# Optimization experiments

Measured on AMD Instinct MI355X. Metric: run time of the kernel, lower is better.

## Reference

```python
import jax, jax.numpy as jnp
import numpy as np

B, N, K, C = 8, 4096, 16, 64
OUT = [128, 128, 128]
BN_EPS = 1e-3


def setup_inputs() -> dict:
    key = jax.random.key(0)
    ks = jax.random.split(key, 8)
    inp = {
        "points1": jax.random.normal(ks[0], (B, 3, N), jnp.float32),
        "points2": jax.random.normal(ks[1], (B, 3, N), jnp.float32),
        "features1": jax.random.normal(ks[2], (B, C, N), jnp.float32),
        "features2": jax.random.normal(ks[3], (B, C, N), jnp.float32),
    }
    dims = [2 * C + 3] + OUT  # [131, 128, 128, 128]
    for i in range(len(OUT)):
        kw = jax.random.fold_in(ks[4], i)
        inp[f"W{i}"] = jax.random.normal(kw, (dims[i + 1], dims[i]), jnp.float32) / np.sqrt(dims[i]).astype(np.float32)
        inp[f"b{i}"] = jnp.zeros((dims[i + 1],), jnp.float32)
        inp[f"gamma{i}"] = jnp.ones((dims[i + 1],), jnp.float32)
        inp[f"beta{i}"] = jnp.zeros((dims[i + 1],), jnp.float32)
    return inp


def _knn_group(points2, points1, features2):
    # points*: [B, 3, N].  For each query in points1, find K nearest in points2.
    d = jnp.sum((points1[:, :, :, None] - points2[:, :, None, :]) ** 2, axis=1)  # [B, Nq, Ns]
    _, idx = jax.lax.top_k(-d, K)  # [B, Nq, K]
    idx_b = idx[:, None, :, :]  # [B, 1, Nq, K] broadcasts over channel dim
    xyz_g = jnp.take_along_axis(points2[:, :, None, :], idx_b, axis=3)      # [B, 3, Nq, K]
    rel_xyz = xyz_g - points1[:, :, :, None]                                # relative coords
    feat_g = jnp.take_along_axis(features2[:, :, None, :], idx_b, axis=3)  # [B, C, Nq, K]
    return jnp.concatenate([rel_xyz, feat_g], axis=1)  # [B, C+3, Nq, K]


def _conv_bn_relu(x, W, b, gamma, beta):
    # 1x1 conv == per-position channel matmul; BN in training mode (batch stats, biased var)
    x = jnp.einsum('oc,bcnk->bonk', W, x) + b[None, :, None, None]
    mu = jnp.mean(x, axis=(0, 2, 3), keepdims=True)
    var = jnp.var(x, axis=(0, 2, 3), keepdims=True)
    x = (x - mu) * jax.lax.rsqrt(var + BN_EPS)
    x = x * gamma[None, :, None, None] + beta[None, :, None, None]
    return jax.nn.relu(x)


def reference(points1, points2, features1, features2,
              W0, b0, gamma0, beta0,
              W1, b1, gamma1, beta1,
              W2, b2, gamma2, beta2):
    g = _knn_group(points2, points1, features2)                       # [B, C+3, N, K]
    f1 = jnp.broadcast_to(features1[:, :, :, None], (B, C, N, K))     # expand over neighbors
    x = jnp.concatenate([g, f1], axis=1)                              # [B, 2C+3, N, K]
    x = _conv_bn_relu(x, W0, b0, gamma0, beta0)
    x = _conv_bn_relu(x, W1, b1, gamma1, beta1)
    x = _conv_bn_relu(x, W2, b2, gamma2, beta2)
    return jnp.max(x, axis=3)                                         # [B, OUT[-1], N]
```

## Files before the change

### kernel.cpp

```cpp
#include <hip/hip_runtime.h>
#include <hip/hip_bf16.h>

#define B_ 8
#define N_ 4096
#define K_ 16
#define C_ 64
#define NK_ (N_*K_)
#define M_ (B_*N_*K_)
#define BN_EPS_ 0.001f
#define Q_ (B_*N_)
#define NB1_ (M_/128)
#define CAP_ 48

typedef short bf16x8 __attribute__((ext_vector_type(8)));
typedef float f32x4 __attribute__((ext_vector_type(4)));

static __device__ __forceinline__ unsigned pk2bf(float a, float b) {
  union { __hip_bfloat162 h; unsigned u; } c;
  c.h = __float22bfloat162_rn(make_float2(a, b));
  return c.u;
}
static __device__ __forceinline__ unsigned short f2bf1(float x) {
  union { __hip_bfloat16 h; unsigned short u; } c;
  c.h = __float2bfloat16(x);
  return c.u;
}

static __device__ __forceinline__ float knn_key(float ax, float ay, float az, float4 c) {
  float dx = ax - c.x, dy = ay - c.y, dz = az - c.z;
  return __fadd_rn(__fadd_rn(__fmul_rn(dx, dx), __fmul_rn(dy, dy)), __fmul_rn(dz, dz));
}

__global__ __launch_bounds__(256) void prep_kernel(
    const float* __restrict__ p1, const float* __restrict__ p2,
    const float* __restrict__ W1, const float* __restrict__ W2,
    const float* __restrict__ W0,
    float4* __restrict__ p1f4, float4* __restrict__ p2f4,
    unsigned short* __restrict__ W1b, unsigned short* __restrict__ W2b,
    float* __restrict__ w0at, float* __restrict__ stats, int* __restrict__ done) {
  int blk = blockIdx.x, tid = threadIdx.x;
  if (blk < 128) {
    int i = blk * 256 + tid;
    int b = i >> 12, n = i & (N_ - 1);
    const float* base = p1 + (size_t)b * 3 * N_;
    p1f4[i] = make_float4(base[n], base[N_ + n], base[2 * N_ + n], 0.f);
  } else if (blk < 256) {
    int i = (blk - 128) * 256 + tid;
    int b = i >> 12, n = i & (N_ - 1);
    const float* base = p2 + (size_t)b * 3 * N_;
    p2f4[i] = make_float4(base[n], base[N_ + n], base[2 * N_ + n], 0.f);
  } else if (blk < 320) {
    int i = (blk - 256) * 256 + tid;
    W1b[i] = f2bf1(W1[i]);
  } else if (blk < 384) {
    int i = (blk - 320) * 256 + tid;
    W2b[i] = f2bf1(W2[i]);
  } else {
    if (tid < 128)
      for (int d = 0; d < 3; ++d) w0at[d * 128 + tid] = W0[tid * 131 + d];
    for (int i = tid; i < 768; i += 256) stats[i] = 0.f;
    if (tid < 3) done[tid] = 0;
  }
}

__global__ __launch_bounds__(64) void knn_sub(const float4* __restrict__ p1f4,
                                              const float4* __restrict__ p2f4,
                                              float* __restrict__ pvals) {
  int lane = threadIdx.x;
  int blk = blockIdx.x;
  int c = blk & 3;
  int grp = (blk >> 2) & 63;
  int b = blk >> 8;
  int q = (b << 12) + (grp << 6) + lane;
  float4 qv = p1f4[q];
  float ax = qv.x, ay = qv.y, az = qv.z;
  const float4* pb = p2f4 + ((size_t)b << 12) + c * 128;

  float s[16];
  #pragma unroll
  for (int i = 0; i < 16; ++i) s[i] = 3.0e38f;

  #pragma unroll 8
  for (int t = 0; t < 128; ++t) {
    float d = knn_key(ax, ay, az, pb[t]);
    #pragma unroll
    for (int i = 0; i < 15; ++i) s[i] = __builtin_amdgcn_fmed3f(s[i], s[i + 1], d);
    s[15] = fminf(s[15], d);
  }
  #pragma unroll
  for (int i = 0; i < 16; ++i) pvals[(size_t)(c * 16 + i) * Q_ + q] = s[i];
}

__global__ __launch_bounds__(64) void knn_t0(const float* __restrict__ pvals,
                                             float* __restrict__ Tarr) {
  int q = blockIdx.x * 64 + threadIdx.x;
  float s[16];
  #pragma unroll
  for (int i = 0; i < 16; ++i) s[i] = 3.0e38f;
  #pragma unroll 8
  for (int t = 0; t < 64; ++t) {
    float d = pvals[(size_t)t * Q_ + q];
    #pragma unroll
    for (int i = 0; i < 15; ++i) s[i] = __builtin_amdgcn_fmed3f(s[i], s[i + 1], d);
    s[15] = fminf(s[15], d);
  }
  Tarr[q] = s[0];
}

__global__ __launch_bounds__(64) void knn_collect(const float4* __restrict__ p1f4,
                                                  const float4* __restrict__ p2f4,
                                                  const float* __restrict__ Tarr,
                                                  uint2* __restrict__ cbuf,
                                                  int* __restrict__ ccnt) {
  int lane = threadIdx.x;
  int blk = blockIdx.x;
  int c = blk & 7;
  int grp = (blk >> 3) & 63;
  int b = blk >> 9;
  int q = (b << 12) + (grp << 6) + lane;
  float4 qv = p1f4[q];
  float ax = qv.x, ay = qv.y, az = qv.z;
  const float4* pb = p2f4 + ((size_t)b << 12) + c * 512;
  float T = Tarr[q];
  uint2* cq = cbuf + (size_t)q * (8 * CAP_) + c * CAP_;
  int cnt = 0;
  #pragma unroll 4
  for (int t = 0; t < 512; ++t) {
    float d = knn_key(ax, ay, az, pb[t]);
    if (d <= T && cnt < CAP_) {
      cq[cnt] = make_uint2(__float_as_uint(d), c * 512 + t);
      ++cnt;
    }
  }
  ccnt[c * Q_ + q] = cnt;
}

__global__ __launch_bounds__(256) void knn_final(const uint2* __restrict__ cbuf,
                                                 const int* __restrict__ ccnt,
                                                 int* __restrict__ idxout) {
  int lane = threadIdx.x & 63;
  int q = blockIdx.x * 4 + (threadIdx.x >> 6);
  const uint2* cq = cbuf + (size_t)q * (8 * CAP_);

  float key[8], okey[8];
  unsigned kidx[8];
  #pragma unroll
  for (int c = 0; c < 8; ++c) {
    int m = ccnt[c * Q_ + q];
    float k = 3.0e38f; unsigned id = 0;
    if (lane < m) {
      uint2 e = cq[c * CAP_ + lane];
      k = __uint_as_float(e.x); id = e.y;
    }
    key[c] = k; okey[c] = k; kidx[c] = id;
  }

  float T = 3.0e38f;
  for (int r = 0; r < 16; ++r) {
    float lm = key[0]; int ls = 0;
    #pragma unroll
    for (int c = 1; c < 8; ++c) if (key[c] < lm) { lm = key[c]; ls = c; }
    float wm = lm;
    wm = fminf(wm, __shfl_xor(wm, 1));
    wm = fminf(wm, __shfl_xor(wm, 2));
    wm = fminf(wm, __shfl_xor(wm, 4));
    wm = fminf(wm, __shfl_xor(wm, 8));
    wm = fminf(wm, __shfl_xor(wm, 16));
    wm = fminf(wm, __shfl_xor(wm, 32));
    T = wm;
    unsigned long long msk = __ballot(lm == wm);
    int owner = __ffsll((long long)msk) - 1;
    if (lane == owner) key[ls] = 3.0e38f;
  }

  int tot = 0, ob = q * 16;
  #pragma unroll
  for (int c = 0; c < 8; ++c) {
    bool take = (okey[c] <= T);
    unsigned long long msk = __ballot(take);
    int pos = tot + __popcll(msk & ((1ull << lane) - 1ull));
    if (take && pos < 16) idxout[ob + pos] = (int)kidx[c];
    tot += __popcll(msk);
  }
}

__global__ __launch_bounds__(256) void pkern(const float* __restrict__ f,
                                             const float* __restrict__ W0,
                                             const float* __restrict__ bias,
                                             const float4* __restrict__ pf4,
                                             const float* __restrict__ w0at,
                                             float sgn,
                                             float* __restrict__ P, int coff) {
  __shared__ float fx[32 * 65];
  __shared__ __align__(16) float Wl[64 * 132];
  int tid = threadIdx.x;
  int bn0 = blockIdx.x * 32;
  int b = bn0 >> 12, nb0 = bn0 & (N_ - 1);

  for (int u = tid; u < 32 * 64; u += 256) {
    int c = u >> 5, nl = u & 31;
    fx[nl * 65 + c] = f[((size_t)b * C_ + c) * N_ + nb0 + nl];
  }
  for (int u = tid; u < 128 * 64; u += 256) {
    int o = u >> 6, c = u & 63;
    Wl[c * 132 + o] = W0[o * 131 + coff + c];
  }
  __syncthreads();

  int og = tid & 15, np_ = tid >> 4;
  int o0 = og * 8;
  int na = np_ * 2, nb = na + 1;
  float acc0[8], acc1[8];
  #pragma unroll
  for (int j = 0; j < 8; ++j) {
    float bv = bias ? bias[o0 + j] : 0.f;
    acc0[j] = bv; acc1[j] = bv;
  }
  for (int c = 0; c < 64; ++c) {
    float x0 = fx[na * 65 + c], x1 = fx[nb * 65 + c];
    float4 wa = *(const float4*)&Wl[c * 132 + o0];
    float4 wb = *(const float4*)&Wl[c * 132 + o0 + 4];
    float w[8] = {wa.x, wa.y, wa.z, wa.w, wb.x, wb.y, wb.z, wb.w};
    #pragma unroll
    for (int j = 0; j < 8; ++j) {
      acc0[j] = fmaf(x0, w[j], acc0[j]);
      acc1[j] = fmaf(x1, w[j], acc1[j]);
    }
  }
  float4 pa = pf4[bn0 + na], pb_ = pf4[bn0 + nb];
  #pragma unroll
  for (int j = 0; j < 8; ++j) {
    float wx = w0at[o0 + j], wy = w0at[128 + o0 + j], wz = w0at[256 + o0 + j];
    acc0[j] += sgn * (wx * pa.x + wy * pa.y + wz * pa.z);
    acc1[j] += sgn * (wx * pb_.x + wy * pb_.y + wz * pb_.z);
  }
  float* Pa = P + (size_t)(bn0 + na) * 128 + o0;
  float* Pb = P + (size_t)(bn0 + nb) * 128 + o0;
  *(float4*)Pa = make_float4(acc0[0], acc0[1], acc0[2], acc0[3]);
  *(float4*)(Pa + 4) = make_float4(acc0[4], acc0[5], acc0[6], acc0[7]);
  *(float4*)Pb = make_float4(acc1[0], acc1[1], acc1[2], acc1[3]);
  *(float4*)(Pb + 4) = make_float4(acc1[4], acc1[5], acc1[6], acc1[7]);
}

__global__ __launch_bounds__(256) void gstats_kernel(
    const float* __restrict__ A, const float* __restrict__ Bv,
    const int* __restrict__ idx, unsigned short* __restrict__ x0b,
    float* __restrict__ part) {
  __shared__ float sred[4 * 128 * 2];
  int tid = threadIdx.x;
  int R0 = blockIdx.x * 128;
  int b = R0 >> 16;
  int n0 = (R0 & (NK_ - 1)) >> 4;
  int cc = (tid & 15) * 8;
  int r0l = tid >> 4;

  int jj[8];
  #pragma unroll
  for (int p = 0; p < 8; ++p) jj[p] = idx[R0 + r0l + p * 16];

  float ssum[8], ssq[8];
  #pragma unroll
  for (int u = 0; u < 8; ++u) { ssum[u] = 0.f; ssq[u] = 0.f; }

  #pragma unroll
  for (int p = 0; p < 8; ++p) {
    const float* Ar = A + (size_t)((b << 12) + n0 + p) * 128 + cc;
    const float* Br = Bv + (size_t)((b << 12) + jj[p]) * 128 + cc;
    float av[8], bv[8];
    *(float4*)&av[0] = *(const float4*)Ar;  *(float4*)&av[4] = *(const float4*)(Ar + 4);
    *(float4*)&bv[0] = *(const float4*)Br;  *(float4*)&bv[4] = *(const float4*)(Br + 4);
    unsigned pw[4];
    #pragma unroll
    for (int i = 0; i < 4; ++i)
      pw[i] = pk2bf(av[2 * i] + bv[2 * i], av[2 * i + 1] + bv[2 * i + 1]);
    uint4 pk; pk.x = pw[0]; pk.y = pw[1]; pk.z = pw[2]; pk.w = pw[3];
    *(uint4*)(x0b + (size_t)(R0 + r0l + p * 16) * 128 + cc) = pk;
    #pragma unroll
    for (int i = 0; i < 4; ++i) {
      float q0 = __uint_as_float(pw[i] << 16);
      float q1 = __uint_as_float(pw[i] & 0xFFFF0000u);
      ssum[2 * i] += q0;     ssq[2 * i] = fmaf(q0, q0, ssq[2 * i]);
      ssum[2 * i + 1] += q1; ssq[2 * i + 1] = fmaf(q1, q1, ssq[2 * i + 1]);
    }
  }
  int w = tid >> 6, lane = tid & 63;
  #pragma unroll
  for (int u = 0; u < 8; ++u) {
    ssum[u] += __shfl_xor(ssum[u], 16);
    ssum[u] += __shfl_xor(ssum[u], 32);
    ssq[u] += __shfl_xor(ssq[u], 16);
    ssq[u] += __shfl_xor(ssq[u], 32);
  }
  if (lane < 16) {
    #pragma unroll
    for (int u = 0; u < 8; ++u) {
      sred[(w * 128 + lane * 8 + u) * 2] = ssum[u];
      sred[(w * 128 + lane * 8 + u) * 2 + 1] = ssq[u];
    }
  }
  __syncthreads();
  if (tid < 128) {
    float a = 0.f, q2 = 0.f;
    #pragma unroll
    for (int ww = 0; ww < 4; ++ww) {
      a += sred[(ww * 128 + tid) * 2];
      q2 += sred[(ww * 128 + tid) * 2 + 1];
    }
    part[(size_t)blockIdx.x * 256 + tid] = a;
    part[(size_t)blockIdx.x * 256 + 128 + tid] = q2;
  }
}

__global__ __launch_bounds__(256) void reduce_bnfin(
    const float* __restrict__ part, float* __restrict__ statso,
    int* __restrict__ done, const float* __restrict__ gamma,
    const float* __restrict__ beta, float* __restrict__ bnp) {
  __shared__ int lastv;
  int tid = threadIdx.x;
  int r0 = blockIdx.x * 16;
  float a = 0.f;
  #pragma unroll
  for (int i = 0; i < 16; ++i) a += part[(size_t)(r0 + i) * 256 + tid];
  atomicAdd(statso + tid, a);
  __threadfence();
  __syncthreads();
  if (tid == 0) lastv = atomicAdd(done, 1);
  __syncthreads();
  if (lastv == (int)gridDim.x - 1) {
    __threadfence();
    if (tid < 128) {
      float s0 = atomicAdd(statso + tid, 0.f);
      float s1 = atomicAdd(statso + 128 + tid, 0.f);
      const float invM = 1.0f / (float)M_;
      float mean = s0 * invM;
      float var = s1 * invM - mean * mean;
      float s = gamma[tid] * rsqrtf(var + BN_EPS_);
      bnp[tid] = s;
      bnp[128 + tid] = beta[tid] - mean * s;
    }
  }
}

static __device__ __forceinline__ char* xsa(unsigned short* Xs, int row, int bytecol) {
  return (char*)Xs + row * 256 + (bytecol ^ ((row & 7) << 4));
}

static __device__ __forceinline__ void stage_lin(
    unsigned short* Xs, const unsigned short* x0b, const float* bnp0,
    int R0, int tid) {
  int cc = (tid & 15) * 8;
  int r0l = tid >> 4;
  float svv[8], tvv[8];
  *(float4*)&svv[0] = *(const float4*)(bnp0 + cc);       *(float4*)&svv[4] = *(const float4*)(bnp0 + cc + 4);
  *(float4*)&tvv[0] = *(const float4*)(bnp0 + 128 + cc); *(float4*)&tvv[4] = *(const float4*)(bnp0 + 132 + cc);
  #pragma unroll
  for (int p = 0; p < 8; ++p) {
    uint4 pv = *(const uint4*)(x0b + (size_t)(R0 + r0l + p * 16) * 128 + cc);
    float xv[8];
    xv[0] = __uint_as_float(pv.x << 16); xv[1] = __uint_as_float(pv.x & 0xFFFF0000u);
    xv[2] = __uint_as_float(pv.y << 16); xv[3] = __uint_as_float(pv.y & 0xFFFF0000u);
    xv[4] = __uint_as_float(pv.z << 16); xv[5] = __uint_as_float(pv.z & 0xFFFF0000u);
    xv[6] = __uint_as_float(pv.w << 16); xv[7] = __uint_as_float(pv.w & 0xFFFF0000u);
    float y[8];
    #pragma unroll
    for (int u = 0; u < 8; ++u) y[u] = fmaxf(fmaf(svv[u], xv[u], tvv[u]), 0.f);
    uint4 pk;
    pk.x = pk2bf(y[0], y[1]); pk.y = pk2bf(y[2], y[3]);
    pk.z = pk2bf(y[4], y[5]); pk.w = pk2bf(y[6], y[7]);
    *(uint4*)xsa(Xs, r0l + p * 16, 16 * (tid & 15)) = pk;
  }
}

__global__ __launch_bounds__(256) void pass1_kernel(
    const unsigned short* __restrict__ x0b, const float* __restrict__ bnp0,
    const unsigned short* __restrict__ W1b, const float* __restrict__ b1,
    float* __restrict__ part) {
  __shared__ __align__(16) unsigned short Xs[128 * 128];
  int tid = threadIdx.x;
  int R0 = blockIdx.x * 128;

  stage_lin(Xs, x0b, bnp0, R0, tid);

  int w = tid >> 6, lane = tid & 63;
  int m16 = lane & 15, qd = lane >> 4;

  bf16x8 bf[2][4];
  #pragma unroll
  for (int nt = 0; nt < 2; ++nt) {
    const unsigned short* wb = W1b + (size_t)(w * 32 + nt * 16 + m16) * 128 + qd * 8;
    #pragma unroll
    for (int q = 0; q < 4; ++q) bf[nt][q] = *(const bf16x8*)(wb + q * 32);
  }
  __syncthreads();

  f32x4 acc[8][2];
  #pragma unroll
  for (int m = 0; m < 8; ++m) {
    acc[m][0] = (f32x4){0.f, 0.f, 0.f, 0.f};
    acc[m][1] = (f32x4){0.f, 0.f, 0.f, 0.f};
  }
  #pragma unroll
  for (int m = 0; m < 8; ++m) {
    bf16x8 a[4];
    #pragma unroll
    for (int q = 0; q < 4; ++q) a[q] = *(const bf16x8*)xsa(Xs, m * 16 + m16, 16 * qd + 64 * q);
    #pragma unroll
    for (int q = 0; q < 4; ++q) {
      acc[m][0] = __builtin_amdgcn_mfma_f32_16x16x32_bf16(a[q], bf[0][q], acc[m][0], 0, 0, 0);
      acc[m][1] = __builtin_amdgcn_mfma_f32_16x16x32_bf16(a[q], bf[1][q], acc[m][1], 0, 0, 0);
    }
  }

  float ssum[2] = {0.f, 0.f}, ssq[2] = {0.f, 0.f};
  #pragma unroll
  for (int nt = 0; nt < 2; ++nt) {
    float bb = b1[w * 32 + nt * 16 + m16];
    #pragma unroll
    for (int m = 0; m < 8; ++m)
      #pragma unroll
      for (int rg = 0; rg < 4; ++rg) {
        float y = acc[m][nt][rg] + bb;
        ssum[nt] += y;
        ssq[nt] = fmaf(y, y, ssq[nt]);
      }
  }
  #pragma unroll
  for (int nt = 0; nt < 2; ++nt) {
    ssum[nt] += __shfl_xor(ssum[nt], 16);
    ssum[nt] += __shfl_xor(ssum[nt], 32);
    ssq[nt] += __shfl_xor(ssq[nt], 16);
    ssq[nt] += __shfl_xor(ssq[nt], 32);
  }
  if (lane < 16) {
    size_t pb = (size_t)blockIdx.x * 256 + w * 32;
    #pragma unroll
    for (int nt = 0; nt < 2; ++nt) {
      part[pb + nt * 16 + lane] = ssum[nt];
      part[pb + 128 + nt * 16 + lane] = ssq[nt];
    }
  }
}

__global__ __launch_bounds__(256) void pass2_kernel(
    const unsigned short* __restrict__ x0b, const float* __restrict__ bnp0,
    const unsigned short* __restrict__ W1b, const float* __restrict__ b1,
    const float* __restrict__ bnp1, const unsigned short* __restrict__ W2b,
    const float* __restrict__ b2, float* __restrict__ ymaxo,
    float* __restrict__ ymino, float* __restrict__ part) {
  __shared__ __align__(16) unsigned short Xs[128 * 128];
  int tid = threadIdx.x;
  int R0 = blockIdx.x * 128;
  int b = R0 >> 16;
  int n0 = (R0 & (NK_ - 1)) >> 4;

  stage_lin(Xs, x0b, bnp0, R0, tid);

  int w = tid >> 6, lane = tid & 63;
  int m16 = lane & 15, qd = lane >> 4;

  bf16x8 bf[2][4];
  #pragma unroll
  for (int nt = 0; nt < 2; ++nt) {
    const unsigned short* wb = W1b + (size_t)(w * 32 + nt * 16 + m16) * 128 + qd * 8;
    #pragma unroll
    for (int q = 0; q < 4; ++q) bf[nt][q] = *(const bf16x8*)(wb + q * 32);
  }
  __syncthreads();

  f32x4 acc[8][2];
  #pragma unroll
  for (int m = 0; m < 8; ++m) {
    acc[m][0] = (f32x4){0.f, 0.f, 0.f, 0.f};
    acc[m][1] = (f32x4){0.f, 0.f, 0.f, 0.f};
  }
  #pragma unroll
  for (int m = 0; m < 8; ++m) {
    bf16x8 a[4];
    #pragma unroll
    for (int q = 0; q < 4; ++q) a[q] = *(const bf16x8*)xsa(Xs, m * 16 + m16, 16 * qd + 64 * q);
    #pragma unroll
    for (int q = 0; q < 4; ++q) {
      acc[m][0] = __builtin_amdgcn_mfma_f32_16x16x32_bf16(a[q], bf[0][q], acc[m][0], 0, 0, 0);
      acc[m][1] = __builtin_amdgcn_mfma_f32_16x16x32_bf16(a[q], bf[1][q], acc[m][1], 0, 0, 0);
    }
  }
  __syncthreads();

  #pragma unroll
  for (int nt = 0; nt < 2; ++nt) {
    int col = w * 32 + nt * 16 + m16;
    float sc = bnp1[col];
    float tc = fmaf(sc, b1[col], bnp1[128 + col]);
    #pragma unroll
    for (int m = 0; m < 8; ++m)
      #pragma unroll
      for (int rg = 0; rg < 4; ++rg) {
        int row = m * 16 + qd * 4 + rg;
        float y = fmaxf(fmaf(sc, acc[m][nt][rg], tc), 0.f);
        *(unsigned short*)xsa(Xs, row, 2 * col) = f2bf1(y);
      }
  }

  bf16x8 bf2[2][4];
  #pragma unroll
  for (int nt = 0; nt < 2; ++nt) {
    const unsigned short* wb = W2b + (size_t)(w * 32 + nt * 16 + m16) * 128 + qd * 8;
    #pragma unroll
    for (int q = 0; q < 4; ++q) bf2[nt][q] = *(const bf16x8*)(wb + q * 32);
  }
  __syncthreads();

  #pragma unroll
  for (int m = 0; m < 8; ++m) {
    acc[m][0] = (f32x4){0.f, 0.f, 0.f, 0.f};
    acc[m][1] = (f32x4){0.f, 0.f, 0.f, 0.f};
  }
  #pragma unroll
  for (int m = 0; m < 8; ++m) {
    bf16x8 a[4];
    #pragma unroll
    for (int q = 0; q < 4; ++q) a[q] = *(const bf16x8*)xsa(Xs, m * 16 + m16, 16 * qd + 64 * q);
    #pragma unroll
    for (int q = 0; q < 4; ++q) {
      acc[m][0] = __builtin_amdgcn_mfma_f32_16x16x32_bf16(a[q], bf2[0][q], acc[m][0], 0, 0, 0);
      acc[m][1] = __builtin_amdgcn_mfma_f32_16x16x32_bf16(a[q], bf2[1][q], acc[m][1], 0, 0, 0);
    }
  }

  float ssum[2] = {0.f, 0.f}, ssq[2] = {0.f, 0.f};
  #pragma unroll
  for (int nt = 0; nt < 2; ++nt) {
    float bb = b2[w * 32 + nt * 16 + m16];
    #pragma unroll
    for (int m = 0; m < 8; ++m) {
      float y0 = acc[m][nt][0] + bb;
      float mx = y0, mn = y0, su = y0, sq = y0 * y0;
      #pragma unroll
      for (int rg = 1; rg < 4; ++rg) {
        float y = acc[m][nt][rg] + bb;
        mx = fmaxf(mx, y); mn = fminf(mn, y);
        su += y; sq = fmaf(y, y, sq);
      }
      mx = fmaxf(mx, __shfl_xor(mx, 16)); mx = fmaxf(mx, __shfl_xor(mx, 32));
      mn = fminf(mn, __shfl_xor(mn, 16)); mn = fminf(mn, __shfl_xor(mn, 32));
      ssum[nt] += su; ssq[nt] += sq;
      if (lane < 16) {
        int n = n0 + m;
        size_t basey = ((size_t)(b << 12) + n) * 128 + w * 32 + nt * 16 + lane;
        ymaxo[basey] = mx;
        ymino[basey] = mn;
      }
    }
  }
  #pragma unroll
  for (int nt = 0; nt < 2; ++nt) {
    ssum[nt] += __shfl_xor(ssum[nt], 16);
    ssum[nt] += __shfl_xor(ssum[nt], 32);
    ssq[nt] += __shfl_xor(ssq[nt], 16);
    ssq[nt] += __shfl_xor(ssq[nt], 32);
  }
  if (lane < 16) {
    size_t pb = (size_t)blockIdx.x * 256 + w * 32;
    #pragma unroll
    for (int nt = 0; nt < 2; ++nt) {
      part[pb + nt * 16 + lane] = ssum[nt];
      part[pb + 128 + nt * 16 + lane] = ssq[nt];
    }
  }
}

__global__ __launch_bounds__(256) void final_kernel(const float* __restrict__ ymaxo,
                                                    const float* __restrict__ ymino,
                                                    const float* __restrict__ bnp2,
                                                    float* __restrict__ out) {
  __shared__ float T[64 * 129];
  int tid = threadIdx.x;
  int b = blockIdx.x >> 6;
  int n0 = (blockIdx.x & 63) * 64;
  for (int u = tid; u < 64 * 128; u += 256) {
    int nl = u >> 7, o = u & 127;
    size_t base = ((size_t)(b << 12) + n0 + nl) * 128 + o;
    float s = bnp2[o], t = bnp2[128 + o];
    float v = fmaf(s, (s >= 0.f ? ymaxo[base] : ymino[base]), t);
    T[nl * 129 + o] = fmaxf(v, 0.f);
  }
  __syncthreads();
  for (int u = tid; u < 64 * 128; u += 256) {
    int o = u >> 6, nl = u & 63;
    out[((size_t)b * 128 + o) * N_ + n0 + nl] = T[nl * 129 + o];
  }
}

extern "C" void kernel_launch(void* const* d_in, const int* in_sizes, int n_in,
                              void* d_out, int out_size, void* d_ws, size_t ws_size,
                              hipStream_t stream) {
  (void)in_sizes; (void)n_in; (void)out_size; (void)ws_size;
  const float* points1 = (const float*)d_in[0];
  const float* points2 = (const float*)d_in[1];
  const float* features1 = (const float*)d_in[2];
  const float* features2 = (const float*)d_in[3];
  const float* W0 = (const float*)d_in[4];
  const float* b0 = (const float*)d_in[5];
  const float* g0 = (const float*)d_in[6];
  const float* be0 = (const float*)d_in[7];
  const float* W1 = (const float*)d_in[8];
  const float* b1 = (const float*)d_in[9];
  const float* g1 = (const float*)d_in[10];
  const float* be1 = (const float*)d_in[11];
  const float* W2 = (const float*)d_in[12];
  const float* b2 = (const float*)d_in[13];
  const float* g2 = (const float*)d_in[14];
  const float* be2 = (const float*)d_in[15];
  float* out = (float*)d_out;

  char* ws = (char*)d_ws;
  size_t off = 0;
  auto alloc = [&](size_t bytes) -> void* {
    void* p = ws + off;
    off += (bytes + 255) & ~(size_t)255;
    return p;
  };
  int* idx = (int*)alloc((size_t)M_ * 4);
  float4* p1f4 = (float4*)alloc((size_t)B_ * N_ * 16);
  float4* p2f4 = (float4*)alloc((size_t)B_ * N_ * 16);
  float* A = (float*)alloc((size_t)B_ * N_ * 128 * 4);
  float* Bv = (float*)alloc((size_t)B_ * N_ * 128 * 4);
  unsigned short* W1b = (unsigned short*)alloc(128 * 128 * 2);
  unsigned short* W2b = (unsigned short*)alloc(128 * 128 * 2);
  float* w0at = (float*)alloc(3 * 128 * 4);
  float* stats = (float*)alloc(3 * 256 * 4);
  float* bnp = (float*)alloc(3 * 256 * 4);
  int* done = (int*)alloc(3 * 4);
  float* ymaxo = (float*)alloc((size_t)B_ * N_ * 128 * 4);
  float* ymino = (float*)alloc((size_t)B_ * N_ * 128 * 4);
  char* bigbuf = (char*)alloc((size_t)128 * 1024 * 1024);
  uint2* cbuf = (uint2*)bigbuf;
  float* pvals = (float*)(bigbuf + (size_t)98 * 1024 * 1024);
  float* Tarr = (float*)(bigbuf + (size_t)107 * 1024 * 1024);
  int* ccnt = (int*)(bigbuf + (size_t)108 * 1024 * 1024);
  unsigned short* x0b = (unsigned short*)bigbuf;

  float* part0 = ymaxo;
  float* part1 = ymino;
  float* part2 = A;

  prep_kernel<<<385, 256, 0, stream>>>(points1, points2, W1, W2, W0,
                                       p1f4, p2f4, W1b, W2b, w0at, stats, done);

  knn_sub<<<B_ * 64 * 4, 64, 0, stream>>>(p1f4, p2f4, pvals);
  knn_t0<<<Q_ / 64, 64, 0, stream>>>(pvals, Tarr);
  knn_collect<<<B_ * 64 * 8, 64, 0, stream>>>(p1f4, p2f4, Tarr, cbuf, ccnt);
  knn_final<<<Q_ / 4, 256, 0, stream>>>(cbuf, ccnt, idx);

  pkern<<<B_ * N_ / 32, 256, 0, stream>>>(features1, W0, b0, p1f4, w0at, -1.f, A, 67);
  pkern<<<B_ * N_ / 32, 256, 0, stream>>>(features2, W0, nullptr, p2f4, w0at, 1.f, Bv, 3);

  gstats_kernel<<<NB1_, 256, 0, stream>>>(A, Bv, idx, x0b, part0);
  reduce_bnfin<<<256, 256, 0, stream>>>(part0, stats, done, g0, be0, bnp);

  pass1_kernel<<<NB1_, 256, 0, stream>>>(x0b, bnp, W1b, b1, part1);
  reduce_bnfin<<<256, 256, 0, stream>>>(part1, stats + 256, done + 1, g1, be1, bnp + 256);

  pass2_kernel<<<NB1_, 256, 0, stream>>>(x0b, bnp, W1b, b1, bnp + 256,
                                         W2b, b2, ymaxo, ymino, part2);
  reduce_bnfin<<<256, 256, 0, stream>>>(part2, stats + 512, done + 2, g2, be2, bnp + 512);

  final_kernel<<<B_ * N_ / 64, 256, 0, stream>>>(ymaxo, ymino, bnp + 512, out);
}
```

Before: 509.1 us.

## Merge KNN partial pass with feature projections and add dot-product prefilter in collect

The knn_sub pass and the two pkern projection launches are combined into one heterogeneous kernel, mega1, whose blocks branch by index. This cuts launch overhead and lets the small KNN work overlap the projection matmuls. knn_collect now uses the precomputed squared norm in the w slot of p2f4 to screen candidates with a cheap dot product before computing the exact distance. The screen uses a 1e-2 slack, which risks missing a true candidate if rounding exceeds that margin, and the merged kernel carries the large shared allocation even on its KNN blocks.

```diff
diff --git a/kernel.cpp b/kernel.cpp
--- a/kernel.cpp
+++ b/kernel.cpp
@@ -43,12 +43,14 @@
     int i = blk * 256 + tid;
     int b = i >> 12, n = i & (N_ - 1);
     const float* base = p1 + (size_t)b * 3 * N_;
-    p1f4[i] = make_float4(base[n], base[N_ + n], base[2 * N_ + n], 0.f);
+    float x = base[n], y = base[N_ + n], z = base[2 * N_ + n];
+    p1f4[i] = make_float4(x, y, z, fmaf(z, z, fmaf(y, y, x * x)));
   } else if (blk < 256) {
     int i = (blk - 128) * 256 + tid;
     int b = i >> 12, n = i & (N_ - 1);
     const float* base = p2 + (size_t)b * 3 * N_;
-    p2f4[i] = make_float4(base[n], base[N_ + n], base[2 * N_ + n], 0.f);
+    float x = base[n], y = base[N_ + n], z = base[2 * N_ + n];
+    p2f4[i] = make_float4(x, y, z, fmaf(z, z, fmaf(y, y, x * x)));
   } else if (blk < 320) {
     int i = (blk - 256) * 256 + tid;
     W1b[i] = f2bf1(W1[i]);
@@ -63,32 +65,101 @@
   }
 }
 
-__global__ __launch_bounds__(64) void knn_sub(const float4* __restrict__ p1f4,
-                                              const float4* __restrict__ p2f4,
-                                              float* __restrict__ pvals) {
-  int lane = threadIdx.x;
+static __device__ __forceinline__ void pkern_body(
+    const float* __restrict__ f, const float* __restrict__ W0,
+    const float* __restrict__ bias, const float4* __restrict__ pf4,
+    const float* __restrict__ w0at, float sgn, float* __restrict__ P,
+    int coff, int blk, float* fx, float* Wl) {
+  int tid = threadIdx.x;
+  int bn0 = blk * 32;
+  int b = bn0 >> 12, nb0 = bn0 & (N_ - 1);
+
+  for (int u = tid; u < 32 * 64; u += 256) {
+    int c = u >> 5, nl = u & 31;
+    fx[nl * 65 + c] = f[((size_t)b * C_ + c) * N_ + nb0 + nl];
+  }
+  for (int u = tid; u < 128 * 64; u += 256) {
+    int o = u >> 6, c = u & 63;
+    Wl[c * 132 + o] = W0[o * 131 + coff + c];
+  }
+  __syncthreads();
+
+  int og = tid & 15, np_ = tid >> 4;
+  int o0 = og * 8;
+  int na = np_ * 2, nb = na + 1;
+  float acc0[8], acc1[8];
+  #pragma unroll
+  for (int j = 0; j < 8; ++j) {
+    float bv = bias ? bias[o0 + j] : 0.f;
+    acc0[j] = bv; acc1[j] = bv;
+  }
+  for (int c = 0; c < 64; ++c) {
+    float x0 = fx[na * 65 + c], x1 = fx[nb * 65 + c];
+    float4 wa = *(const float4*)&Wl[c * 132 + o0];
+    float4 wb = *(const float4*)&Wl[c * 132 + o0 + 4];
+    float w[8] = {wa.x, wa.y, wa.z, wa.w, wb.x, wb.y, wb.z, wb.w};
+    #pragma unroll
+    for (int j = 0; j < 8; ++j) {
+      acc0[j] = fmaf(x0, w[j], acc0[j]);
+      acc1[j] = fmaf(x1, w[j], acc1[j]);
+    }
+  }
+  float4 pa = pf4[bn0 + na], pb_ = pf4[bn0 + nb];
+  #pragma unroll
+  for (int j = 0; j < 8; ++j) {
+    float wx = w0at[o0 + j], wy = w0at[128 + o0 + j], wz = w0at[256 + o0 + j];
+    acc0[j] += sgn * (wx * pa.x + wy * pa.y + wz * pa.z);
+    acc1[j] += sgn * (wx * pb_.x + wy * pb_.y + wz * pb_.z);
+  }
+  float* Pa = P + (size_t)(bn0 + na) * 128 + o0;
+  float* Pb = P + (size_t)(bn0 + nb) * 128 + o0;
+  *(float4*)Pa = make_float4(acc0[0], acc0[1], acc0[2], acc0[3]);
+  *(float4*)(Pa + 4) = make_float4(acc0[4], acc0[5], acc0[6], acc0[7]);
+  *(float4*)Pb = make_float4(acc1[0], acc1[1], acc1[2], acc1[3]);
+  *(float4*)(Pb + 4) = make_float4(acc1[4], acc1[5], acc1[6], acc1[7]);
+}
+
+__global__ __launch_bounds__(256) void mega1(
+    const float4* __restrict__ p1f4, const float4* __restrict__ p2f4,
+    float* __restrict__ pvals,
+    const float* __restrict__ f1, const float* __restrict__ f2,
+    const float* __restrict__ W0, const float* __restrict__ b0,
+    const float* __restrict__ w0at, float* __restrict__ A,
+    float* __restrict__ Bv) {
+  __shared__ __align__(16) float smem[32 * 65 + 64 * 132];
   int blk = blockIdx.x;
-  int c = blk & 3;
-  int grp = (blk >> 2) & 63;
-  int b = blk >> 8;
-  int q = (b << 12) + (grp << 6) + lane;
-  float4 qv = p1f4[q];
-  float ax = qv.x, ay = qv.y, az = qv.z;
-  const float4* pb = p2f4 + ((size_t)b << 12) + c * 128;
-
-  float s[16];
-  #pragma unroll
-  for (int i = 0; i < 16; ++i) s[i] = 3.0e38f;
-
-  #pragma unroll 8
-  for (int t = 0; t < 128; ++t) {
-    float d = knn_key(ax, ay, az, pb[t]);
-    #pragma unroll
-    for (int i = 0; i < 15; ++i) s[i] = __builtin_amdgcn_fmed3f(s[i], s[i + 1], d);
-    s[15] = fminf(s[15], d);
-  }
-  #pragma unroll
-  for (int i = 0; i < 16; ++i) pvals[(size_t)(c * 16 + i) * Q_ + q] = s[i];
+  if (blk < 512) {
+    int tid = threadIdx.x;
+    int lane = tid & 63;
+    int oblk = blk * 4 + (tid >> 6);
+    int c = oblk & 3;
+    int grp = (oblk >> 2) & 63;
+    int b = oblk >> 8;
+    int q = (b << 12) + (grp << 6) + lane;
+    float4 qv = p1f4[q];
+    float ax = qv.x, ay = qv.y, az = qv.z;
+    const float4* pb = p2f4 + ((size_t)b << 12) + c * 128;
+
+    float s[16];
+    #pragma unroll
+    for (int i = 0; i < 16; ++i) s[i] = 3.0e38f;
+
+    #pragma unroll 8
+    for (int t = 0; t < 128; ++t) {
+      float d = knn_key(ax, ay, az, pb[t]);
+      #pragma unroll
+      for (int i = 0; i < 15; ++i) s[i] = __builtin_amdgcn_fmed3f(s[i], s[i + 1], d);
+      s[15] = fminf(s[15], d);
+    }
+    #pragma unroll
+    for (int i = 0; i < 16; ++i) pvals[(size_t)(c * 16 + i) * Q_ + q] = s[i];
+  } else if (blk < 1536) {
+    pkern_body(f1, W0, b0, p1f4, w0at, -1.f, A, 67, blk - 512,
+               smem, smem + 32 * 65);
+  } else {
+    pkern_body(f2, W0, nullptr, p2f4, w0at, 1.f, Bv, 3, blk - 1536,
+               smem, smem + 32 * 65);
+  }
 }
 
 __global__ __launch_bounds__(64) void knn_t0(const float* __restrict__ pvals,
@@ -122,14 +193,20 @@
   float ax = qv.x, ay = qv.y, az = qv.z;
   const float4* pb = p2f4 + ((size_t)b << 12) + c * 512;
   float T = Tarr[q];
+  float Tscr = T - qv.w + 1e-2f;
   uint2* cq = cbuf + (size_t)q * (8 * CAP_) + c * CAP_;
   int cnt = 0;
   #pragma unroll 4
   for (int t = 0; t < 512; ++t) {
-    float d = knn_key(ax, ay, az, pb[t]);
-    if (d <= T && cnt < CAP_) {
-      cq[cnt] = make_uint2(__float_as_uint(d), c * 512 + t);
-      ++cnt;
+    float4 cd = pb[t];
+    float dotv = fmaf(az, cd.z, fmaf(ay, cd.y, ax * cd.x));
+    float dscr = fmaf(-2.f, dotv, cd.w);
+    if (dscr <= Tscr) {
+      float d = knn_key(ax, ay, az, cd);
+      if (d <= T && cnt < CAP_) {
+        cq[cnt] = make_uint2(__float_as_uint(d), c * 512 + t);
+        ++cnt;
+      }
     }
   }
   ccnt[c * Q_ + q] = cnt;
@@ -182,64 +259,6 @@
     if (take && pos < 16) idxout[ob + pos] = (int)kidx[c];
     tot += __popcll(msk);
   }
-}
-
-__global__ __launch_bounds__(256) void pkern(const float* __restrict__ f,
-                                             const float* __restrict__ W0,
-                                             const float* __restrict__ bias,
-                                             const float4* __restrict__ pf4,
-                                             const float* __restrict__ w0at,
-                                             float sgn,
-                                             float* __restrict__ P, int coff) {
-  __shared__ float fx[32 * 65];
-  __shared__ __align__(16) float Wl[64 * 132];
-  int tid = threadIdx.x;
-  int bn0 = blockIdx.x * 32;
-  int b = bn0 >> 12, nb0 = bn0 & (N_ - 1);
-
-  for (int u = tid; u < 32 * 64; u += 256) {
-    int c = u >> 5, nl = u & 31;
-    fx[nl * 65 + c] = f[((size_t)b * C_ + c) * N_ + nb0 + nl];
-  }
-  for (int u = tid; u < 128 * 64; u += 256) {
-    int o = u >> 6, c = u & 63;
-    Wl[c * 132 + o] = W0[o * 131 + coff + c];
-  }
-  __syncthreads();
-
-  int og = tid & 15, np_ = tid >> 4;
-  int o0 = og * 8;
-  int na = np_ * 2, nb = na + 1;
-  float acc0[8], acc1[8];
-  #pragma unroll
-  for (int j = 0; j < 8; ++j) {
-    float bv = bias ? bias[o0 + j] : 0.f;
-    acc0[j] = bv; acc1[j] = bv;
-  }
-  for (int c = 0; c < 64; ++c) {
-    float x0 = fx[na * 65 + c], x1 = fx[nb * 65 + c];
-    float4 wa = *(const float4*)&Wl[c * 132 + o0];
-    float4 wb = *(const float4*)&Wl[c * 132 + o0 + 4];
-    float w[8] = {wa.x, wa.y, wa.z, wa.w, wb.x, wb.y, wb.z, wb.w};
-    #pragma unroll
-    for (int j = 0; j < 8; ++j) {
-      acc0[j] = fmaf(x0, w[j], acc0[j]);
-      acc1[j] = fmaf(x1, w[j], acc1[j]);
-    }
-  }
-  float4 pa = pf4[bn0 + na], pb_ = pf4[bn0 + nb];
-  #pragma unroll
-  for (int j = 0; j < 8; ++j) {
-    float wx = w0at[o0 + j], wy = w0at[128 + o0 + j], wz = w0at[256 + o0 + j];
-    acc0[j] += sgn * (wx * pa.x + wy * pa.y + wz * pa.z);
-    acc1[j] += sgn * (wx * pb_.x + wy * pb_.y + wz * pb_.z);
-  }
-  float* Pa = P + (size_t)(bn0 + na) * 128 + o0;
-  float* Pb = P + (size_t)(bn0 + nb) * 128 + o0;
-  *(float4*)Pa = make_float4(acc0[0], acc0[1], acc0[2], acc0[3]);
-  *(float4*)(Pa + 4) = make_float4(acc0[4], acc0[5], acc0[6], acc0[7]);
-  *(float4*)Pb = make_float4(acc1[0], acc1[1], acc1[2], acc1[3]);
-  *(float4*)(Pb + 4) = make_float4(acc1[4], acc1[5], acc1[6], acc1[7]);
 }
 
 __global__ __launch_bounds__(256) void gstats_kernel(
@@ -647,14 +666,13 @@
   prep_kernel<<<385, 256, 0, stream>>>(points1, points2, W1, W2, W0,
                                        p1f4, p2f4, W1b, W2b, w0at, stats, done);
 
-  knn_sub<<<B_ * 64 * 4, 64, 0, stream>>>(p1f4, p2f4, pvals);
+  mega1<<<2560, 256, 0, stream>>>(p1f4, p2f4, pvals, features1, features2,
+                                  W0, b0, w0at, A, Bv);
+
   knn_t0<<<Q_ / 64, 64, 0, stream>>>(pvals, Tarr);
   knn_collect<<<B_ * 64 * 8, 64, 0, stream>>>(p1f4, p2f4, Tarr, cbuf, ccnt);
   knn_final<<<Q_ / 4, 256, 0, stream>>>(cbuf, ccnt, idx);
 
-  pkern<<<B_ * N_ / 32, 256, 0, stream>>>(features1, W0, b0, p1f4, w0at, -1.f, A, 67);
-  pkern<<<B_ * N_ / 32, 256, 0, stream>>>(features2, W0, nullptr, p2f4, w0at, 1.f, Bv, 3);
-
   gstats_kernel<<<NB1_, 256, 0, stream>>>(A, Bv, idx, x0b, part0);
   reduce_bnfin<<<256, 256, 0, stream>>>(part0, stats, done, g0, be0, bnp);
 
```

After: 498.9 us. 2.0% less time.
